# Kernel optimization log

Hardware: AMD Instinct MI355X
Metric: run time of the kernel (lower is better)

Reference implementation:

```python
import jax, jax.numpy as jnp
import numpy as np

COST_CLASS = 1.0
COST_POLYLINE = 1.0
NUM_QUERIES, BS, NUM_CLASSES = 100, 8, 4
N_PTS, N_TGT = 30, 512


def setup_inputs() -> dict:
    key = jax.random.key(0)
    k1, k2, k3, k4 = jax.random.split(key, 4)
    return {
        "pred_logits": jax.random.normal(k1, (NUM_QUERIES, BS, NUM_CLASSES), dtype=jnp.float32),
        "pred_polylines": jax.random.normal(k2, (NUM_QUERIES, BS, N_PTS, 2), dtype=jnp.float32),
        "tgt_ids": jax.random.randint(k3, (N_TGT,), 0, NUM_CLASSES, dtype=jnp.int32),
        "tgt_polylines": jax.random.normal(k4, (N_TGT, N_PTS, 2), dtype=jnp.float32),
    }


def reference(pred_logits, pred_polylines, tgt_ids, tgt_polylines):
    nq, bs, nc = pred_logits.shape
    # flatten(0,1): [nq*bs, C] / [nq*bs, n_pts, 2]
    out_prob = jax.nn.softmax(pred_logits.reshape(nq * bs, nc), axis=-1)
    out_poly = pred_polylines.reshape(nq * bs, -1, 2)

    # classification cost: -p(target class), [P, T]
    cost_class = -out_prob[:, tgt_ids]

    # pairwise symmetric chamfer with L1 point distance.
    # D[p, t, i, j] = ||out_poly[p, i] - tgt_polylines[t, j]||_1  -> [P, T, np, nt]
    D = jnp.abs(out_poly[:, None, :, None, :] - tgt_polylines[None, :, None, :, :]).sum(-1)
    min1 = D.min(axis=3).mean(axis=2)  # pred -> tgt
    min2 = D.min(axis=2).mean(axis=2)  # tgt -> pred
    cost_polyline = (min1 + min2) * 0.5

    C = COST_CLASS * cost_class + COST_POLYLINE * cost_polyline
    # original does C.view(bs, num_queries, -1) on the (nq, bs)-flattened axis;
    # replicate that exact memory reinterpretation.
    return C.reshape(bs, nq, -1)
```

## Files before the change

kernel.cpp:

```cpp
#include <hip/hip_runtime.h>
#include <math.h>

#define NQ      100
#define BS      8
#define NC      4
#define NPTS    30
#define NTGT    512
#define P_TOTAL (NQ*BS)
#define TILE_P  8
#define TILE_T  64
#define NTHREADS 512

typedef float        f32x2 __attribute__((ext_vector_type(2)));
typedef unsigned int u32x2 __attribute__((ext_vector_type(2)));

__device__ __forceinline__ f32x2 pksub_sv(u32x2 sp, f32x2 t) {
    f32x2 r;
    asm("v_pk_add_f32 %0, %1, %2 neg_lo:[0,1] neg_hi:[0,1]"
        : "=v"(r) : "s"(sp), "v"(t));
    return r;
}
__device__ __forceinline__ float maxabs2(f32x2 w) {
    float d;
    asm("v_max_f32 %0, abs(%1), abs(%2)" : "=v"(d) : "v"(w.x), "v"(w.y));
    return d;
}
__device__ __forceinline__ float min3f(float a, float b, float c) {
    float r;
    asm("v_min3_f32 %0, %1, %2, %3" : "=v"(r) : "v"(a), "v"(b), "v"(c));
    return r;
}

__global__ __launch_bounds__(NTHREADS) void matcher_kernel(
    const float* __restrict__ logits,
    const float* __restrict__ pred_poly,
    const int*   __restrict__ tgt_ids,
    const float* __restrict__ tgt_poly,
    float*       __restrict__ out)
{
    __shared__ f32x2 srt_t[NPTS][TILE_T + 1];
    __shared__ float prob_lds[TILE_P][NC];

    const int tid = threadIdx.x;
    const int p0  = blockIdx.x * TILE_P;
    const int t0  = blockIdx.y * TILE_T;

    for (int idx = tid; idx < TILE_T * NPTS; idx += NTHREADS) {
        const int tt = idx / NPTS;
        const int j  = idx - tt * NPTS;
        const float2 v = *reinterpret_cast<const float2*>(
            tgt_poly + (size_t)(t0 + tt) * (NPTS * 2) + j * 2);
        srt_t[j][tt] = f32x2{v.x + v.y, v.x - v.y};
    }
    if (tid < TILE_P) {
        const float* l = logits + (size_t)(p0 + tid) * NC;
        const float a0 = l[0], a1 = l[1], a2 = l[2], a3 = l[3];
        const float m  = fmaxf(fmaxf(a0, a1), fmaxf(a2, a3));
        const float e0 = expf(a0 - m), e1 = expf(a1 - m);
        const float e2 = expf(a2 - m), e3 = expf(a3 - m);
        const float inv = 1.0f / (e0 + e1 + e2 + e3);
        prob_lds[tid][0] = e0 * inv;
        prob_lds[tid][1] = e1 * inv;
        prob_lds[tid][2] = e2 * inv;
        prob_lds[tid][3] = e3 * inv;
    }

    const int w  = tid >> 6;
    const int tl = tid & 63;

    u32x2 sp[NPTS];
    {
        const float2* pp = reinterpret_cast<const float2*>(
            pred_poly + (size_t)(p0 + w) * (NPTS * 2));
#pragma unroll
        for (int i = 0; i < NPTS; ++i) {
            const float2 v = pp[i];
            sp[i].x = __builtin_amdgcn_readfirstlane(__float_as_uint(v.x + v.y));
            sp[i].y = __builtin_amdgcn_readfirstlane(__float_as_uint(v.x - v.y));
        }
    }
    __syncthreads();

    float m1[NPTS];
#pragma unroll
    for (int i = 0; i < NPTS; ++i) m1[i] = 1e30f;

    float sum2 = 0.0f;
#pragma unroll 1
    for (int j2 = 0; j2 < NPTS / 2; ++j2) {
        const f32x2 tv0 = srt_t[2 * j2][tl];
        const f32x2 tv1 = srt_t[2 * j2 + 1][tl];
        float dj0 = 1e30f, dj1 = 1e30f;
#pragma unroll
        for (int i = 0; i < NPTS; i += 2) {
            const float d00 = maxabs2(pksub_sv(sp[i],     tv0));
            const float d01 = maxabs2(pksub_sv(sp[i],     tv1));
            const float d10 = maxabs2(pksub_sv(sp[i + 1], tv0));
            const float d11 = maxabs2(pksub_sv(sp[i + 1], tv1));
            m1[i]     = min3f(m1[i],     d00, d01);
            m1[i + 1] = min3f(m1[i + 1], d10, d11);
            dj0       = min3f(dj0, d00, d10);
            dj1       = min3f(dj1, d01, d11);
        }
        sum2 += dj0 + dj1;
    }

    float sum1 = 0.0f;
#pragma unroll
    for (int i = 0; i < NPTS; ++i) sum1 += m1[i];

    const int   t   = t0 + tl;
    const int   cls = tgt_ids[t];
    const float cc  = -prob_lds[w][cls];
    out[(size_t)(p0 + w) * NTGT + t] = cc + (sum1 + sum2) * (0.5f / (float)NPTS);
}

extern "C" void kernel_launch(void* const* d_in, const int* in_sizes, int n_in,
                              void* d_out, int out_size, void* d_ws, size_t ws_size,
                              hipStream_t stream) {
    const float* logits    = (const float*)d_in[0];
    const float* pred_poly = (const float*)d_in[1];
    const int*   tids      = (const int*)d_in[2];
    const float* tgt_poly  = (const float*)d_in[3];
    float*       out       = (float*)d_out;

    dim3 grid(P_TOTAL / TILE_P, NTGT / TILE_T);
    dim3 block(NTHREADS);
    matcher_kernel<<<grid, block, 0, stream>>>(logits, pred_poly, tids, tgt_poly, out);
}
```

Baseline: 49.01 us.

## Split each target's points across two lanes with shuffle-based reduction

Each (pred, target) pair is now handled by two lanes, each covering half of the target points (15 each), and the partial row minima and column sums are combined with xor shuffles. Block and tile sizes shrink (4 preds × 32 targets, 256 threads), so the grid has four times as many blocks, which is meant to improve occupancy and latency hiding on a grid that was small for the GPU. The cost is 30 extra shuffles per thread, an odd leftover point handled outside the paired loop, and half the lanes idle during the output store.

```diff
diff --git a/kernel.cpp b/kernel.cpp
--- a/kernel.cpp
+++ b/kernel.cpp
@@ -5,11 +5,12 @@
 #define BS      8
 #define NC      4
 #define NPTS    30
+#define JH      15
 #define NTGT    512
 #define P_TOTAL (NQ*BS)
-#define TILE_P  8
-#define TILE_T  64
-#define NTHREADS 512
+#define TILE_P  4
+#define TILE_T  32
+#define NTHREADS 256
 
 typedef float        f32x2 __attribute__((ext_vector_type(2)));
 typedef unsigned int u32x2 __attribute__((ext_vector_type(2)));
@@ -38,7 +39,7 @@
     const float* __restrict__ tgt_poly,
     float*       __restrict__ out)
 {
-    __shared__ f32x2 srt_t[NPTS][TILE_T + 1];
+    __shared__ f32x2 srt[NPTS][TILE_T + 1];
     __shared__ float prob_lds[TILE_P][NC];
 
     const int tid = threadIdx.x;
@@ -50,7 +51,7 @@
         const int j  = idx - tt * NPTS;
         const float2 v = *reinterpret_cast<const float2*>(
             tgt_poly + (size_t)(t0 + tt) * (NPTS * 2) + j * 2);
-        srt_t[j][tt] = f32x2{v.x + v.y, v.x - v.y};
+        srt[j][tt] = f32x2{v.x + v.y, v.x - v.y};
     }
     if (tid < TILE_P) {
         const float* l = logits + (size_t)(p0 + tid) * NC;
@@ -65,8 +66,10 @@
         prob_lds[tid][3] = e3 * inv;
     }
 
-    const int w  = tid >> 6;
-    const int tl = tid & 63;
+    const int w    = tid >> 6;
+    const int lane = tid & 63;
+    const int t    = lane >> 1;
+    const int jb   = (lane & 1) * JH;
 
     u32x2 sp[NPTS];
     {
@@ -87,9 +90,9 @@
 
     float sum2 = 0.0f;
 #pragma unroll 1
-    for (int j2 = 0; j2 < NPTS / 2; ++j2) {
-        const f32x2 tv0 = srt_t[2 * j2][tl];
-        const f32x2 tv1 = srt_t[2 * j2 + 1][tl];
+    for (int jp = 0; jp < JH / 2; ++jp) {
+        const f32x2 tv0 = srt[jb + 2 * jp][t];
+        const f32x2 tv1 = srt[jb + 2 * jp + 1][t];
         float dj0 = 1e30f, dj1 = 1e30f;
 #pragma unroll
         for (int i = 0; i < NPTS; i += 2) {
@@ -104,15 +107,34 @@
         }
         sum2 += dj0 + dj1;
     }
+    {
+        const f32x2 tv0 = srt[jb + JH - 1][t];
+        float dj0 = 1e30f;
+#pragma unroll
+        for (int i = 0; i < NPTS; i += 2) {
+            const float d00 = maxabs2(pksub_sv(sp[i],     tv0));
+            const float d10 = maxabs2(pksub_sv(sp[i + 1], tv0));
+            m1[i]     = fminf(m1[i],     d00);
+            m1[i + 1] = fminf(m1[i + 1], d10);
+            dj0       = min3f(dj0, d00, d10);
+        }
+        sum2 += dj0;
+    }
 
+    sum2 += __shfl_xor(sum2, 1, 64);
     float sum1 = 0.0f;
 #pragma unroll
-    for (int i = 0; i < NPTS; ++i) sum1 += m1[i];
+    for (int i = 0; i < NPTS; ++i) {
+        const float o = __shfl_xor(m1[i], 1, 64);
+        sum1 += fminf(m1[i], o);
+    }
 
-    const int   t   = t0 + tl;
-    const int   cls = tgt_ids[t];
-    const float cc  = -prob_lds[w][cls];
-    out[(size_t)(p0 + w) * NTGT + t] = cc + (sum1 + sum2) * (0.5f / (float)NPTS);
+    if ((lane & 1) == 0) {
+        const int   tg  = t0 + t;
+        const int   cls = tgt_ids[tg];
+        const float cc  = -prob_lds[w][cls];
+        out[(size_t)(p0 + w) * NTGT + tg] = cc + (sum1 + sum2) * (0.5f / (float)NPTS);
+    }
 }
 
 extern "C" void kernel_launch(void* const* d_in, const int* in_sizes, int n_in,
```

Result: faster. 47.36 us (-3.4%).

## Stage predicted polylines in LDS and halve block tile to four predictions

Applied to the files above, without the earlier changes.

Predicted polyline points are no longer held in scalar registers via readfirstlane. They are now precomputed into a shared-memory array and read as broadcast LDS loads inside the inner loop. The block also shrinks from 8 to 4 predictions (256 threads), which doubles the grid and lowers per-block LDS and register pressure. In exchange, the inner loop gains LDS reads where it previously used SGPR operands, and each target tile is reloaded by twice as many blocks.

```diff
diff --git a/kernel.cpp b/kernel.cpp
--- a/kernel.cpp
+++ b/kernel.cpp
@@ -7,17 +7,16 @@
 #define NPTS    30
 #define NTGT    512
 #define P_TOTAL (NQ*BS)
-#define TILE_P  8
+#define TILE_P  4
 #define TILE_T  64
-#define NTHREADS 512
+#define NTHREADS 256
 
-typedef float        f32x2 __attribute__((ext_vector_type(2)));
-typedef unsigned int u32x2 __attribute__((ext_vector_type(2)));
+typedef float f32x2 __attribute__((ext_vector_type(2)));
 
-__device__ __forceinline__ f32x2 pksub_sv(u32x2 sp, f32x2 t) {
+__device__ __forceinline__ f32x2 pksub(f32x2 p, f32x2 t) {
     f32x2 r;
     asm("v_pk_add_f32 %0, %1, %2 neg_lo:[0,1] neg_hi:[0,1]"
-        : "=v"(r) : "s"(sp), "v"(t));
+        : "=v"(r) : "v"(p), "v"(t));
     return r;
 }
 __device__ __forceinline__ float maxabs2(f32x2 w) {
@@ -39,6 +38,7 @@
     float*       __restrict__ out)
 {
     __shared__ f32x2 srt_t[NPTS][TILE_T + 1];
+    __shared__ f32x2 srt_p[TILE_P][NPTS];
     __shared__ float prob_lds[TILE_P][NC];
 
     const int tid = threadIdx.x;
@@ -52,6 +52,13 @@
             tgt_poly + (size_t)(t0 + tt) * (NPTS * 2) + j * 2);
         srt_t[j][tt] = f32x2{v.x + v.y, v.x - v.y};
     }
+    if (tid < TILE_P * NPTS) {
+        const int pp = tid / NPTS;
+        const int i  = tid - pp * NPTS;
+        const float2 v = *reinterpret_cast<const float2*>(
+            pred_poly + (size_t)(p0 + pp) * (NPTS * 2) + i * 2);
+        srt_p[pp][i] = f32x2{v.x + v.y, v.x - v.y};
+    }
     if (tid < TILE_P) {
         const float* l = logits + (size_t)(p0 + tid) * NC;
         const float a0 = l[0], a1 = l[1], a2 = l[2], a3 = l[3];
@@ -64,22 +71,10 @@
         prob_lds[tid][2] = e2 * inv;
         prob_lds[tid][3] = e3 * inv;
     }
+    __syncthreads();
 
-    const int w  = tid >> 6;
-    const int tl = tid & 63;
-
-    u32x2 sp[NPTS];
-    {
-        const float2* pp = reinterpret_cast<const float2*>(
-            pred_poly + (size_t)(p0 + w) * (NPTS * 2));
-#pragma unroll
-        for (int i = 0; i < NPTS; ++i) {
-            const float2 v = pp[i];
-            sp[i].x = __builtin_amdgcn_readfirstlane(__float_as_uint(v.x + v.y));
-            sp[i].y = __builtin_amdgcn_readfirstlane(__float_as_uint(v.x - v.y));
-        }
-    }
-    __syncthreads();
+    const int w    = tid >> 6;
+    const int lane = tid & 63;
 
     float m1[NPTS];
 #pragma unroll
@@ -87,16 +82,18 @@
 
     float sum2 = 0.0f;
 #pragma unroll 1
-    for (int j2 = 0; j2 < NPTS / 2; ++j2) {
-        const f32x2 tv0 = srt_t[2 * j2][tl];
-        const f32x2 tv1 = srt_t[2 * j2 + 1][tl];
+    for (int jp = 0; jp < NPTS / 2; ++jp) {
+        const f32x2 tv0 = srt_t[2 * jp][lane];
+        const f32x2 tv1 = srt_t[2 * jp + 1][lane];
         float dj0 = 1e30f, dj1 = 1e30f;
 #pragma unroll
         for (int i = 0; i < NPTS; i += 2) {
-            const float d00 = maxabs2(pksub_sv(sp[i],     tv0));
-            const float d01 = maxabs2(pksub_sv(sp[i],     tv1));
-            const float d10 = maxabs2(pksub_sv(sp[i + 1], tv0));
-            const float d11 = maxabs2(pksub_sv(sp[i + 1], tv1));
+            const f32x2 sp0 = srt_p[w][i];
+            const f32x2 sp1 = srt_p[w][i + 1];
+            const float d00 = maxabs2(pksub(sp0, tv0));
+            const float d01 = maxabs2(pksub(sp0, tv1));
+            const float d10 = maxabs2(pksub(sp1, tv0));
+            const float d11 = maxabs2(pksub(sp1, tv1));
             m1[i]     = min3f(m1[i],     d00, d01);
             m1[i + 1] = min3f(m1[i + 1], d10, d11);
             dj0       = min3f(dj0, d00, d10);
@@ -109,7 +106,7 @@
 #pragma unroll
     for (int i = 0; i < NPTS; ++i) sum1 += m1[i];
 
-    const int   t   = t0 + tl;
+    const int   t   = t0 + lane;
     const int   cls = tgt_ids[t];
     const float cc  = -prob_lds[w][cls];
     out[(size_t)(p0 + w) * NTGT + t] = cc + (sum1 + sum2) * (0.5f / (float)NPTS);
```

After: 46.55 us. 1.05x faster.
